# Performance work log

Measured on AMD Instinct MI355X. Metric: run time of the kernel, lower is better.

Reference implementation:

```python
import jax, jax.numpy as jnp
import numpy as np

N = 50000
E = 800000
DIN = 128
# SAGEConv layer dims: (in, out). conv0: input->embed; hidden: 128->64->128->256->512
DIMS = [(128, 128), (128, 64), (64, 128), (128, 256), (256, 512)]
NUM_CLASSES = 4


def setup_inputs() -> dict:
    key = jax.random.key(0)
    ks = jax.random.split(key, 3 * len(DIMS) + 4)
    inp = {"x": jax.random.normal(ks[0], (N, DIN), dtype=jnp.float32)}
    for i, (din, dout) in enumerate(DIMS):
        s = 1.0 / np.sqrt(din).astype(np.float32)
        inp[f"Wl{i}"] = jax.random.normal(ks[1 + 3 * i], (dout, din), dtype=jnp.float32) * s
        inp[f"bl{i}"] = jnp.zeros((dout,), dtype=jnp.float32)
        inp[f"Wr{i}"] = jax.random.normal(ks[2 + 3 * i], (dout, din), dtype=jnp.float32) * s
    dlast = DIMS[-1][1]
    inp["Wout"] = jax.random.normal(ks[-2], (NUM_CLASSES, dlast), dtype=jnp.float32) * (1.0 / np.sqrt(dlast).astype(np.float32))
    inp["bout"] = jnp.zeros((NUM_CLASSES,), dtype=jnp.float32)
    inp["edge_index"] = jax.random.randint(ks[-1], (2, E), 0, N, dtype=jnp.int32)
    return inp


def _forward(x, params, edge_index):
    src, dst = edge_index[0], edge_index[1]
    n = x.shape[0]
    # in-degree (count of incoming edges), clamped to >= 1 as in PyG mean aggregation
    deg = jax.ops.segment_sum(jnp.ones((src.shape[0],), x.dtype), dst, num_segments=n)
    deg_inv = (1.0 / jnp.maximum(deg, 1.0))[:, None]

    def sage(h, Wl, bl, Wr):
        # mean aggregation over incoming neighbors, then lin_l(agg) + lin_r(h)
        agg = jax.ops.segment_sum(h[src], dst, num_segments=n) * deg_inv
        return agg @ Wl.T + bl + h @ Wr.T

    h = x
    for i in range(len(DIMS)):
        h = jax.nn.relu(sage(h, params[f"Wl{i}"], params[f"bl{i}"], params[f"Wr{i}"]))
    logits = h @ params["Wout"].T + params["bout"]
    return jax.nn.softmax(logits, axis=-1)


def reference(x, Wl0, bl0, Wr0, Wl1, bl1, Wr1, Wl2, bl2, Wr2, Wl3, bl3, Wr3,
              Wl4, bl4, Wr4, Wout, bout, edge_index):
    params = {"Wl0": Wl0, "bl0": bl0, "Wr0": Wr0, "Wl1": Wl1, "bl1": bl1, "Wr1": Wr1,
              "Wl2": Wl2, "bl2": bl2, "Wr2": Wr2, "Wl3": Wl3, "bl3": bl3, "Wr3": Wr3,
              "Wl4": Wl4, "bl4": bl4, "Wr4": Wr4, "Wout": Wout, "bout": bout}
    return _forward(x, params, edge_index)
```

## Files before the change

kernel.cpp:

```cpp
#include <hip/hip_runtime.h>
#include <hip/hip_bf16.h>
#include <cstdint>
#include <cstddef>


typedef short bf16x8 __attribute__((ext_vector_type(8)));
typedef float f32x16 __attribute__((ext_vector_type(16)));

static inline int idiv_up(int a, int b) { return (a + b - 1) / b; }

static __device__ __forceinline__ float bf2f(unsigned short u) {
  union { unsigned int i; float f; } v; v.i = ((unsigned int)u) << 16; return v.f;
}
static __device__ __forceinline__ unsigned short f2bf(float f) {
  union { float f; unsigned int i; } v; v.f = f;
  return (unsigned short)((v.i + 0x7FFFu + ((v.i >> 16) & 1u)) >> 16);
}
static __device__ __forceinline__ float lo16(unsigned int u) { return bf2f((unsigned short)(u & 0xffffu)); }
static __device__ __forceinline__ float hi16(unsigned int u) { return bf2f((unsigned short)(u >> 16)); }
static __device__ __forceinline__ unsigned int packbf(float a, float b) {
  return (unsigned int)f2bf(a) | ((unsigned int)f2bf(b) << 16);
}

static __device__ __forceinline__ void gl_lds16(const void* g, void* l) {
  typedef __attribute__((address_space(3))) unsigned int lds_u32;
  typedef __attribute__((address_space(1))) const unsigned int glb_u32;
  __builtin_amdgcn_global_load_lds((glb_u32*)(uintptr_t)g,
                                   (lds_u32*)(unsigned int)(uintptr_t)l, 16, 0, 0);
}

__global__ void k_count_deg(const int* __restrict__ dst, int* __restrict__ deg, int E) {
  int e = blockIdx.x * blockDim.x + threadIdx.x;
  if (e < E) atomicAdd(deg + dst[e], 1);
}

__global__ __launch_bounds__(1024)
void k_scan(const int* __restrict__ deg, int* __restrict__ row_off, int* __restrict__ cursor,
            float* __restrict__ deg_inv, int n) {
  __shared__ int wsum[16];
  const int tid = threadIdx.x;
  const int lane = tid & 63, wid = tid >> 6;
  int carry = 0;
  for (int base = 0; base < n; base += 1024) {
    const int i = base + tid;
    const int v = (i < n) ? deg[i] : 0;
    int incl = v;
#pragma unroll
    for (int off = 1; off < 64; off <<= 1) {
      int t = __shfl_up(incl, off);
      if (lane >= off) incl += t;
    }
    if (lane == 63) wsum[wid] = incl;
    __syncthreads();
    if (wid == 0) {
      int wv = (lane < 16) ? wsum[lane] : 0;
#pragma unroll
      for (int off = 1; off < 16; off <<= 1) {
        int t = __shfl_up(wv, off);
        if (lane >= off) wv += t;
      }
      if (lane < 16) wsum[lane] = wv;
    }
    __syncthreads();
    const int woff = (wid > 0) ? wsum[wid - 1] : 0;
    if (i < n) {
      const int ro = carry + woff + incl - v;
      row_off[i] = ro;
      cursor[i] = ro;
      deg_inv[i] = 1.0f / (float)((v > 1) ? v : 1);
    }
    const int tot = wsum[15];
    __syncthreads();
    carry += tot;
  }
  if (tid == 0) row_off[n] = carry;
}

__global__ void k_fill_csr(const int* __restrict__ src, const int* __restrict__ dst,
                           int* __restrict__ cursor, int* __restrict__ esrc, int E) {
  int e = blockIdx.x * blockDim.x + threadIdx.x;
  if (e < E) {
    int d = dst[e];
    int p = atomicAdd(cursor + d, 1);
    esrc[p] = src[e];
  }
}

__global__ __launch_bounds__(256)
void k_conv_x(const float* __restrict__ src, unsigned short* __restrict__ dst, int n4) {
  for (int i = blockIdx.x * blockDim.x + threadIdx.x; i < n4; i += gridDim.x * blockDim.x) {
    const float4 v = *((const float4*)src + i);
    uint2 o;
    o.x = packbf(v.x, v.y);
    o.y = packbf(v.z, v.w);
    *((uint2*)dst + i) = o;
  }
}

struct PackJob { const float* src; unsigned short* dst; int O; int K; };
struct PackJobs { PackJob j[10]; };

__global__ __launch_bounds__(256)
void k_pack_w(PackJobs jobs) {
  const PackJob J = jobs.j[blockIdx.y];
  const int total = J.O * J.K / 2;
  const int OK64 = J.O * 64;
  for (int u = blockIdx.x * blockDim.x + threadIdx.x; u < total; u += gridDim.x * blockDim.x) {
    const int e = u * 2;
    const int kt = e / OK64;
    const int rem = e - kt * OK64;
    const int chunk = rem / (J.O * 8);
    const int rem2 = rem - chunk * (J.O * 8);
    const int col = rem2 >> 3;
    const int j = rem2 & 7;
    const int korig = kt * 64 + chunk * 8 + j;
    const float f0 = J.src[(size_t)col * J.K + korig];
    const float f1 = J.src[(size_t)col * J.K + korig + 1];
    ((unsigned int*)J.dst)[u] = packbf(f0, f1);
  }
}

static __device__ __forceinline__ void acc_u4(float* acc, const uint4& v) {
  acc[0] += lo16(v.x); acc[1] += hi16(v.x);
  acc[2] += lo16(v.y); acc[3] += hi16(v.y);
  acc[4] += lo16(v.z); acc[5] += hi16(v.z);
  acc[6] += lo16(v.w); acc[7] += hi16(v.w);
}

__global__ __launch_bounds__(256)
void k_agg128(const unsigned short* __restrict__ h, const int* __restrict__ row_off,
              const int* __restrict__ esrc, const float* __restrict__ deg_inv,
              unsigned short* __restrict__ agg, int N) {
  const int node = blockIdx.x * 4 + (threadIdx.x >> 6);
  if (node >= N) return;
  const int lane = threadIdx.x & 63;
  const int g = lane >> 4, c = lane & 15;
  const int s0 = row_off[node], s1 = row_off[node + 1];
  const uint4* hp = (const uint4*)h;
  float acc[8] = {0.f, 0.f, 0.f, 0.f, 0.f, 0.f, 0.f, 0.f};
  for (int i = s0; i < s1; i += 16) {
    int el = i + (lane & 15);
    if (el >= s1) el = s1 - 1;
    const int ev = esrc[el];
    uint4 v[4];
#pragma unroll
    for (int u = 0; u < 4; ++u) {
      if (i + u * 4 < s1) {
        const int e = __shfl(ev, u * 4 + g);
        v[u] = hp[(size_t)e * 16 + c];
      }
    }
#pragma unroll
    for (int u = 0; u < 4; ++u)
      if (i + u * 4 + g < s1) acc_u4(acc, v[u]);
  }
#pragma unroll
  for (int j = 0; j < 8; ++j) {
    acc[j] += __shfl_xor(acc[j], 16);
    acc[j] += __shfl_xor(acc[j], 32);
  }
  if (g == 0) {
    const float di = deg_inv[node];
    uint4 o;
    o.x = packbf(acc[0] * di, acc[1] * di);
    o.y = packbf(acc[2] * di, acc[3] * di);
    o.z = packbf(acc[4] * di, acc[5] * di);
    o.w = packbf(acc[6] * di, acc[7] * di);
    ((uint4*)agg)[(size_t)node * 16 + c] = o;
  }
}

__global__ __launch_bounds__(256)
void k_agg256(const unsigned short* __restrict__ h, const int* __restrict__ row_off,
              const int* __restrict__ esrc, const float* __restrict__ deg_inv,
              unsigned short* __restrict__ agg, int N) {
  const int node = blockIdx.x * 4 + (threadIdx.x >> 6);
  if (node >= N) return;
  const int lane = threadIdx.x & 63;
  const int g = lane >> 5, c = lane & 31;
  const int s0 = row_off[node], s1 = row_off[node + 1];
  const uint4* hp = (const uint4*)h;
  float acc[8] = {0.f, 0.f, 0.f, 0.f, 0.f, 0.f, 0.f, 0.f};
  for (int i = s0; i < s1; i += 16) {
    int el = i + (lane & 15);
    if (el >= s1) el = s1 - 1;
    const int ev = esrc[el];
    uint4 v[8];
#pragma unroll
    for (int u = 0; u < 8; ++u) {
      if (i + u * 2 < s1) {
        const int e = __shfl(ev, u * 2 + g);
        v[u] = hp[(size_t)e * 32 + c];
      }
    }
#pragma unroll
    for (int u = 0; u < 8; ++u)
      if (i + u * 2 + g < s1) acc_u4(acc, v[u]);
  }
#pragma unroll
  for (int j = 0; j < 8; ++j) acc[j] += __shfl_xor(acc[j], 32);
  if (g == 0) {
    const float di = deg_inv[node];
    uint4 o;
    o.x = packbf(acc[0] * di, acc[1] * di);
    o.y = packbf(acc[2] * di, acc[3] * di);
    o.z = packbf(acc[4] * di, acc[5] * di);
    o.w = packbf(acc[6] * di, acc[7] * di);
    ((uint4*)agg)[(size_t)node * 32 + c] = o;
  }
}

__global__ __launch_bounds__(256)
void k_agg64(const unsigned short* __restrict__ h, const int* __restrict__ row_off,
             const int* __restrict__ esrc, const float* __restrict__ deg_inv,
             unsigned short* __restrict__ agg, int N) {
  const int node = blockIdx.x * 4 + (threadIdx.x >> 6);
  if (node >= N) return;
  const int lane = threadIdx.x & 63;
  const int g = lane >> 3, c = lane & 7;
  const int s0 = row_off[node], s1 = row_off[node + 1];
  const uint4* hp = (const uint4*)h;
  float acc[8] = {0.f, 0.f, 0.f, 0.f, 0.f, 0.f, 0.f, 0.f};
  for (int i = s0; i < s1; i += 16) {
    int el = i + (lane & 15);
    if (el >= s1) el = s1 - 1;
    const int ev = esrc[el];
    uint4 v[2];
#pragma unroll
    for (int u = 0; u < 2; ++u) {
      if (i + u * 8 < s1) {
        const int e = __shfl(ev, u * 8 + g);
        v[u] = hp[(size_t)e * 8 + c];
      }
    }
#pragma unroll
    for (int u = 0; u < 2; ++u)
      if (i + u * 8 + g < s1) acc_u4(acc, v[u]);
  }
#pragma unroll
  for (int j = 0; j < 8; ++j) {
    acc[j] += __shfl_xor(acc[j], 8);
    acc[j] += __shfl_xor(acc[j], 16);
    acc[j] += __shfl_xor(acc[j], 32);
  }
  if (g == 0) {
    const float di = deg_inv[node];
    uint4 o;
    o.x = packbf(acc[0] * di, acc[1] * di);
    o.y = packbf(acc[2] * di, acc[3] * di);
    o.z = packbf(acc[4] * di, acc[5] * di);
    o.w = packbf(acc[6] * di, acc[7] * di);
    ((uint4*)agg)[(size_t)node * 8 + c] = o;
  }
}

template <int WC>
__global__ __launch_bounds__(WC * 128)
void k_sage_gemm(const unsigned short* __restrict__ A0, const unsigned short* __restrict__ B0,
                 const unsigned short* __restrict__ A1, const unsigned short* __restrict__ B1,
                 const float* __restrict__ bias, unsigned short* __restrict__ C,
                 int Nn, int K, int O) {
  constexpr int BN = WC * 64;
  constexpr int T = WC * 128;
  constexpr int ACH = 1024;
  constexpr int BCH = BN * 8;
  constexpr int LPT = (ACH + BCH) / T;
  constexpr int BSH = (WC == 1) ? 6 : ((WC == 2) ? 7 : 8);
  constexpr int LDSBUF = 16384 + BN * 128;
  __shared__ char lds[2 * LDSBUF];

  const int tid = threadIdx.x;
  const int w = tid >> 6, lane = tid & 63;
  const int wr = w / WC, wc = w % WC;
  const int fr = lane & 31, fq = lane >> 5;
  const int rowp = blockIdx.y;
  const int row0 = rowp * 128 + wr * 64;
  const int colb = blockIdx.x * BN;

  const int KT0 = K >> 6;
  const int NT = 2 * KT0;

  f32x16 acc[2][2];
#pragma unroll
  for (int m = 0; m < 2; ++m)
#pragma unroll
    for (int cn = 0; cn < 2; ++cn)
#pragma unroll
      for (int r = 0; r < 16; ++r) acc[m][cn][r] = 0.f;

  auto stage = [&](int buf, int t) {
    const int ph = (t >= KT0) ? 1 : 0;
    const unsigned short* Ab = ph ? A1 : A0;
    const unsigned short* Bb = ph ? B1 : B0;
    const int ktl = t - ph * KT0;
    char* lb = lds + buf * LDSBUF;
#pragma unroll
    for (int i = 0; i < LPT; ++i) {
      const int ch = tid + i * T;
      if (ch < ACH) {
        const int ar = ch >> 3, s = ch & 7;
        int g = rowp * 128 + ar;
        if (g >= Nn) g = Nn - 1;
        gl_lds16(Ab + (size_t)g * K + ktl * 64 + ((s ^ (ar & 7)) << 3), lb + ch * 16);
      } else {
        const int cb = ch - ACH;
        const int chunk = cb >> BSH, colrel = cb & (BN - 1);
        gl_lds16(Bb + (size_t)ktl * O * 64 + chunk * O * 8 + (colb + colrel) * 8,
                 lb + 16384 + cb * 16);
      }
    }
  };

  stage(0, 0);
#pragma unroll 1
  for (int t = 0; t < NT; ++t) {
    asm volatile("s_waitcnt vmcnt(0)" ::: "memory");
    __syncthreads();
    if (t + 1 < NT) stage((t + 1) & 1, t + 1);
    const char* lb = lds + (t & 1) * LDSBUF;
#pragma unroll
    for (int k16i = 0; k16i < 4; ++k16i) {
      const int c = k16i * 2 + fq;
      bf16x8 af[2], bg[2];
#pragma unroll
      for (int m = 0; m < 2; ++m) {
        const int rl = wr * 64 + m * 32 + fr;
        af[m] = *(const bf16x8*)(lb + rl * 128 + ((c ^ (rl & 7)) << 4));
      }
#pragma unroll
      for (int cn = 0; cn < 2; ++cn) {
        const int colrel = wc * 64 + cn * 32 + fr;
        bg[cn] = *(const bf16x8*)(lb + 16384 + c * (BN * 16) + colrel * 16);
      }
#pragma unroll
      for (int m = 0; m < 2; ++m)
#pragma unroll
        for (int cn = 0; cn < 2; ++cn)
          acc[m][cn] = __builtin_amdgcn_mfma_f32_32x32x16_bf16(af[m], bg[cn], acc[m][cn], 0, 0, 0);
    }
  }

#pragma unroll
  for (int cn = 0; cn < 2; ++cn) {
    const int col = colb + wc * 64 + cn * 32 + fr;
    const float bb = bias[col];
#pragma unroll
    for (int m = 0; m < 2; ++m) {
#pragma unroll
      for (int reg = 0; reg < 16; ++reg) {
        const float v = fmaxf(acc[m][cn][reg] + bb, 0.f);
        const float nb = __shfl_xor(v, 1);
        const int row = row0 + m * 32 + (reg & 3) + 8 * (reg >> 2) + 4 * fq;
        if (!(lane & 1) && row < Nn) {
          *(unsigned int*)(C + (size_t)row * O + col) = packbf(v, nb);
        }
      }
    }
  }
}

__global__ __launch_bounds__(256)
void k_out_softmax(const unsigned short* __restrict__ h, const float* __restrict__ W4,
                   const float* __restrict__ b, float* __restrict__ out, int N) {
  const int n = blockIdx.x * 4 + (threadIdx.x >> 6);
  if (n >= N) return;
  const int lane = threadIdx.x & 63;
  const unsigned int* hp = (const unsigned int*)h + (size_t)n * 256;
  float a[4] = {0.f, 0.f, 0.f, 0.f};
#pragma unroll
  for (int it = 0; it < 4; ++it) {
    const unsigned int v = hp[it * 64 + lane];
    const float lo = lo16(v);
    const float hi = hi16(v);
    const int k = (it * 64 + lane) * 2;
#pragma unroll
    for (int c = 0; c < 4; ++c)
      a[c] += lo * W4[c * 512 + k] + hi * W4[c * 512 + k + 1];
  }
#pragma unroll
  for (int off = 32; off > 0; off >>= 1) {
#pragma unroll
    for (int c = 0; c < 4; ++c) a[c] += __shfl_down(a[c], off);
  }
  if (lane == 0) {
    const float l0 = a[0] + b[0], l1 = a[1] + b[1], l2 = a[2] + b[2], l3 = a[3] + b[3];
    const float m = fmaxf(fmaxf(l0, l1), fmaxf(l2, l3));
    const float e0 = expf(l0 - m), e1 = expf(l1 - m), e2 = expf(l2 - m), e3 = expf(l3 - m);
    const float inv = 1.0f / (e0 + e1 + e2 + e3);
    float4 r; r.x = e0 * inv; r.y = e1 * inv; r.z = e2 * inv; r.w = e3 * inv;
    *(float4*)(out + (size_t)n * 4) = r;
  }
}

extern "C" void kernel_launch(void* const* d_in, const int* in_sizes, int n_in,
                              void* d_out, int out_size, void* d_ws, size_t ws_size,
                              hipStream_t stream) {
  const float* x = (const float*)d_in[0];
  const float* Wl[5] = {(const float*)d_in[1], (const float*)d_in[4], (const float*)d_in[7],
                        (const float*)d_in[10], (const float*)d_in[13]};
  const float* bl[5] = {(const float*)d_in[2], (const float*)d_in[5], (const float*)d_in[8],
                        (const float*)d_in[11], (const float*)d_in[14]};
  const float* Wr[5] = {(const float*)d_in[3], (const float*)d_in[6], (const float*)d_in[9],
                        (const float*)d_in[12], (const float*)d_in[15]};
  const float* Wout = (const float*)d_in[16];
  const float* bout = (const float*)d_in[17];
  const int* eidx = (const int*)d_in[18];

  const int N = in_sizes[0] / 128;
  const int E = in_sizes[18] / 2;
  const int* srcI = eidx;
  const int* dstI = eidx + E;

  const int Kd[5] = {128, 128, 64, 128, 256};
  const int Od[5] = {128, 64, 128, 256, 512};

  char* ws = (char*)d_ws;
  size_t p = 0;
  auto alloc = [&](size_t bytes) { size_t r = p; p += (bytes + 255) & ~(size_t)255; return r; };
  int*   deg     = (int*)(ws + alloc((size_t)N * 4));
  int*   row_off = (int*)(ws + alloc((size_t)(N + 1) * 4));
  int*   cursor  = (int*)(ws + alloc((size_t)N * 4));
  float* deg_inv = (float*)(ws + alloc((size_t)N * 4));
  int*   esrc    = (int*)(ws + alloc((size_t)E * 4));
  unsigned short* xb = (unsigned short*)(ws + alloc((size_t)N * 128 * 2));
  unsigned short* wlb[5];
  unsigned short* wrb[5];
  for (int l = 0; l < 5; ++l) {
    wlb[l] = (unsigned short*)(ws + alloc((size_t)Od[l] * Kd[l] * 2));
    wrb[l] = (unsigned short*)(ws + alloc((size_t)Od[l] * Kd[l] * 2));
  }
  unsigned short* bufA = (unsigned short*)(ws + alloc((size_t)N * 512 * 2));
  unsigned short* bufB = (unsigned short*)(ws + alloc((size_t)N * 256 * 2));
  unsigned short* agg  = (unsigned short*)(ws + alloc((size_t)N * 256 * 2));
  (void)ws_size; (void)n_in; (void)out_size;

  k_conv_x<<<128, 256, 0, stream>>>(x, xb, N * 128 / 4);
  PackJobs jobs;
  for (int l = 0; l < 5; ++l) {
    jobs.j[2 * l]     = {Wl[l], wlb[l], Od[l], Kd[l]};
    jobs.j[2 * l + 1] = {Wr[l], wrb[l], Od[l], Kd[l]};
  }
  k_pack_w<<<dim3(32, 10), 256, 0, stream>>>(jobs);

  hipMemsetAsync(deg, 0, (size_t)N * 4, stream);
  k_count_deg<<<idiv_up(E, 256), 256, 0, stream>>>(dstI, deg, E);
  k_scan<<<1, 1024, 0, stream>>>(deg, row_off, cursor, deg_inv, N);
  k_fill_csr<<<idiv_up(E, 256), 256, 0, stream>>>(srcI, dstI, cursor, esrc, E);

  unsigned short* houts[5] = {bufA, bufB, bufA, bufB, bufA};

  const unsigned short* hin = xb;
  const int gx = idiv_up(N, 128);
  for (int l = 0; l < 5; ++l) {
    const int K = Kd[l], O = Od[l];
    if (K == 64)
      k_agg64<<<idiv_up(N, 4), 256, 0, stream>>>(hin, row_off, esrc, deg_inv, agg, N);
    else if (K == 128)
      k_agg128<<<idiv_up(N, 4), 256, 0, stream>>>(hin, row_off, esrc, deg_inv, agg, N);
    else
      k_agg256<<<idiv_up(N, 4), 256, 0, stream>>>(hin, row_off, esrc, deg_inv, agg, N);

    unsigned short* hout = houts[l];
    switch (l) {
      case 0:
        k_sage_gemm<2><<<dim3(1, gx), 256, 0, stream>>>(agg, wlb[l], hin, wrb[l], bl[l], hout, N, K, O);
        break;
      case 1:
        k_sage_gemm<1><<<dim3(1, gx), 128, 0, stream>>>(agg, wlb[l], hin, wrb[l], bl[l], hout, N, K, O);
        break;
      case 2:
        k_sage_gemm<2><<<dim3(1, gx), 256, 0, stream>>>(agg, wlb[l], hin, wrb[l], bl[l], hout, N, K, O);
        break;
      case 3:
        k_sage_gemm<2><<<dim3(2, gx), 256, 0, stream>>>(agg, wlb[l], hin, wrb[l], bl[l], hout, N, K, O);
        break;
      default:
        k_sage_gemm<2><<<dim3(4, gx), 256, 0, stream>>>(agg, wlb[l], hin, wrb[l], bl[l], hout, N, K, O);
        break;
    }
    hin = hout;
  }
  k_out_softmax<<<idiv_up(N, 4), 256, 0, stream>>>(hin, Wout, bout, (float*)d_out, N);
}
```

Measured before the change: 465.3 us.

## Reorder layer 1 to transform-then-aggregate and remap GEMM blocks for L2 locality

For the 128->64 layer, the code now multiplies h by the concatenated [Wl|Wr] weights first, producing a 128-wide intermediate. A new fused kernel then aggregates the 64-wide Wl·h half over neighbours, scales by deg_inv, and adds the Wr·h half, bias and ReLU. This halves the gathered feature width for that layer, at the cost of an extra GEMM output round trip and bf16 rounding of the pre-aggregated product. The GEMM grid also becomes 1D with a swizzle that groups 8 row tiles across all column blocks, aiming to improve reuse of the A tiles in L2.

```diff
diff --git a/kernel.cpp b/kernel.cpp
--- a/kernel.cpp
+++ b/kernel.cpp
@@ -97,26 +97,22 @@
   }
 }
 
-struct PackJob { const float* src; unsigned short* dst; int O; int K; };
+struct PackJob { const float* src; unsigned short* dst; int O; int K; int colOff; int Opack; };
 struct PackJobs { PackJob j[10]; };
 
 __global__ __launch_bounds__(256)
 void k_pack_w(PackJobs jobs) {
   const PackJob J = jobs.j[blockIdx.y];
   const int total = J.O * J.K / 2;
-  const int OK64 = J.O * 64;
   for (int u = blockIdx.x * blockDim.x + threadIdx.x; u < total; u += gridDim.x * blockDim.x) {
     const int e = u * 2;
-    const int kt = e / OK64;
-    const int rem = e - kt * OK64;
-    const int chunk = rem / (J.O * 8);
-    const int rem2 = rem - chunk * (J.O * 8);
-    const int col = rem2 >> 3;
-    const int j = rem2 & 7;
-    const int korig = kt * 64 + chunk * 8 + j;
-    const float f0 = J.src[(size_t)col * J.K + korig];
-    const float f1 = J.src[(size_t)col * J.K + korig + 1];
-    ((unsigned int*)J.dst)[u] = packbf(f0, f1);
+    const int col = e / J.K;
+    const int k = e - col * J.K;
+    const int kt = k >> 6, ch = (k >> 3) & 7, j = k & 7;
+    const float f0 = J.src[(size_t)col * J.K + k];
+    const float f1 = J.src[(size_t)col * J.K + k + 1];
+    const int didx = kt * (J.Opack * 64) + ch * (J.Opack * 8) + (col + J.colOff) * 8 + j;
+    ((unsigned int*)J.dst)[didx >> 1] = packbf(f0, f1);
   }
 }
 
@@ -254,7 +250,59 @@
   }
 }
 
-template <int WC>
+__global__ __launch_bounds__(256)
+void k_agg_post64(const unsigned short* __restrict__ z, const int* __restrict__ row_off,
+                  const int* __restrict__ esrc, const float* __restrict__ deg_inv,
+                  const float* __restrict__ bias, unsigned short* __restrict__ out, int N) {
+  const int node = blockIdx.x * 4 + (threadIdx.x >> 6);
+  if (node >= N) return;
+  const int lane = threadIdx.x & 63;
+  const int g = lane >> 3, c = lane & 7;
+  const int s0 = row_off[node], s1 = row_off[node + 1];
+  const uint4* zp = (const uint4*)z;
+  float acc[8] = {0.f, 0.f, 0.f, 0.f, 0.f, 0.f, 0.f, 0.f};
+  for (int i = s0; i < s1; i += 16) {
+    int el = i + (lane & 15);
+    if (el >= s1) el = s1 - 1;
+    const int ev = esrc[el];
+    uint4 v[2];
+#pragma unroll
+    for (int u = 0; u < 2; ++u) {
+      if (i + u * 8 < s1) {
+        const int e = __shfl(ev, u * 8 + g);
+        v[u] = zp[(size_t)e * 16 + c];
+      }
+    }
+#pragma unroll
+    for (int u = 0; u < 2; ++u)
+      if (i + u * 8 + g < s1) acc_u4(acc, v[u]);
+  }
+#pragma unroll
+  for (int j = 0; j < 8; ++j) {
+    acc[j] += __shfl_xor(acc[j], 8);
+    acc[j] += __shfl_xor(acc[j], 16);
+    acc[j] += __shfl_xor(acc[j], 32);
+  }
+  if (g == 0) {
+    const float di = deg_inv[node];
+    const uint4 yr = zp[(size_t)node * 16 + 8 + c];
+    float y[8];
+    y[0] = lo16(yr.x); y[1] = hi16(yr.x); y[2] = lo16(yr.y); y[3] = hi16(yr.y);
+    y[4] = lo16(yr.z); y[5] = hi16(yr.z); y[6] = lo16(yr.w); y[7] = hi16(yr.w);
+    float r[8];
+#pragma unroll
+    for (int j = 0; j < 8; ++j)
+      r[j] = fmaxf(acc[j] * di + y[j] + bias[c * 8 + j], 0.f);
+    uint4 o;
+    o.x = packbf(r[0], r[1]);
+    o.y = packbf(r[2], r[3]);
+    o.z = packbf(r[4], r[5]);
+    o.w = packbf(r[6], r[7]);
+    ((uint4*)out)[(size_t)node * 8 + c] = o;
+  }
+}
+
+template <int WC, int NCB, bool FUSED>
 __global__ __launch_bounds__(WC * 128)
 void k_sage_gemm(const unsigned short* __restrict__ A0, const unsigned short* __restrict__ B0,
                  const unsigned short* __restrict__ A1, const unsigned short* __restrict__ B1,
@@ -269,16 +317,23 @@
   constexpr int LDSBUF = 16384 + BN * 128;
   __shared__ char lds[2 * LDSBUF];
 
+  const int nrp = (Nn + 127) >> 7;
+  const int bid = blockIdx.x;
+  const int r8 = bid & 7;
+  const int tb = bid >> 3;
+  const int cb = tb % NCB;
+  const int rowp = (tb / NCB) * 8 + r8;
+  if (rowp >= nrp) return;
+
   const int tid = threadIdx.x;
   const int w = tid >> 6, lane = tid & 63;
   const int wr = w / WC, wc = w % WC;
   const int fr = lane & 31, fq = lane >> 5;
-  const int rowp = blockIdx.y;
   const int row0 = rowp * 128 + wr * 64;
-  const int colb = blockIdx.x * BN;
+  const int colb = cb * BN;
 
   const int KT0 = K >> 6;
-  const int NT = 2 * KT0;
+  const int NT = FUSED ? 2 * KT0 : KT0;
 
   f32x16 acc[2][2];
 #pragma unroll
@@ -289,10 +344,17 @@
       for (int r = 0; r < 16; ++r) acc[m][cn][r] = 0.f;
 
   auto stage = [&](int buf, int t) {
-    const int ph = (t >= KT0) ? 1 : 0;
-    const unsigned short* Ab = ph ? A1 : A0;
-    const unsigned short* Bb = ph ? B1 : B0;
-    const int ktl = t - ph * KT0;
+    const unsigned short* Ab;
+    const unsigned short* Bb;
+    int ktl;
+    if (FUSED) {
+      const int ph = (t >= KT0) ? 1 : 0;
+      Ab = ph ? A1 : A0;
+      Bb = ph ? B1 : B0;
+      ktl = t - ph * KT0;
+    } else {
+      Ab = A0; Bb = B0; ktl = t;
+    }
     char* lb = lds + buf * LDSBUF;
 #pragma unroll
     for (int i = 0; i < LPT; ++i) {
@@ -303,10 +365,10 @@
         if (g >= Nn) g = Nn - 1;
         gl_lds16(Ab + (size_t)g * K + ktl * 64 + ((s ^ (ar & 7)) << 3), lb + ch * 16);
       } else {
-        const int cb = ch - ACH;
-        const int chunk = cb >> BSH, colrel = cb & (BN - 1);
+        const int cbch = ch - ACH;
+        const int chunk = cbch >> BSH, colrel = cbch & (BN - 1);
         gl_lds16(Bb + (size_t)ktl * O * 64 + chunk * O * 8 + (colb + colrel) * 8,
-                 lb + 16384 + cb * 16);
+                 lb + 16384 + cbch * 16);
       }
     }
   };
@@ -343,12 +405,14 @@
 #pragma unroll
   for (int cn = 0; cn < 2; ++cn) {
     const int col = colb + wc * 64 + cn * 32 + fr;
-    const float bb = bias[col];
+    float bb = 0.f;
+    if (FUSED) bb = bias[col];
 #pragma unroll
     for (int m = 0; m < 2; ++m) {
 #pragma unroll
       for (int reg = 0; reg < 16; ++reg) {
-        const float v = fmaxf(acc[m][cn][reg] + bb, 0.f);
+        float v = acc[m][cn][reg];
+        if (FUSED) v = fmaxf(v + bb, 0.f);
         const float nb = __shfl_xor(v, 1);
         const int row = row0 + m * 32 + (reg & 3) + 8 * (reg >> 2) + 4 * fq;
         if (!(lane & 1) && row < Nn) {
@@ -429,6 +493,7 @@
     wlb[l] = (unsigned short*)(ws + alloc((size_t)Od[l] * Kd[l] * 2));
     wrb[l] = (unsigned short*)(ws + alloc((size_t)Od[l] * Kd[l] * 2));
   }
+  unsigned short* wcat1 = (unsigned short*)(ws + alloc((size_t)128 * 128 * 2));
   unsigned short* bufA = (unsigned short*)(ws + alloc((size_t)N * 512 * 2));
   unsigned short* bufB = (unsigned short*)(ws + alloc((size_t)N * 256 * 2));
   unsigned short* agg  = (unsigned short*)(ws + alloc((size_t)N * 256 * 2));
@@ -437,8 +502,13 @@
   k_conv_x<<<128, 256, 0, stream>>>(x, xb, N * 128 / 4);
   PackJobs jobs;
   for (int l = 0; l < 5; ++l) {
-    jobs.j[2 * l]     = {Wl[l], wlb[l], Od[l], Kd[l]};
-    jobs.j[2 * l + 1] = {Wr[l], wrb[l], Od[l], Kd[l]};
+    if (l == 1) {
+      jobs.j[2] = {Wl[1], wcat1, 64, 128, 0, 128};
+      jobs.j[3] = {Wr[1], wcat1, 64, 128, 64, 128};
+    } else {
+      jobs.j[2 * l]     = {Wl[l], wlb[l], Od[l], Kd[l], 0, Od[l]};
+      jobs.j[2 * l + 1] = {Wr[l], wrb[l], Od[l], Kd[l], 0, Od[l]};
+    }
   }
   k_pack_w<<<dim3(32, 10), 256, 0, stream>>>(jobs);
 
@@ -447,38 +517,22 @@
   k_scan<<<1, 1024, 0, stream>>>(deg, row_off, cursor, deg_inv, N);
   k_fill_csr<<<idiv_up(E, 256), 256, 0, stream>>>(srcI, dstI, cursor, esrc, E);
 
-  unsigned short* houts[5] = {bufA, bufB, bufA, bufB, bufA};
-
-  const unsigned short* hin = xb;
-  const int gx = idiv_up(N, 128);
-  for (int l = 0; l < 5; ++l) {
-    const int K = Kd[l], O = Od[l];
-    if (K == 64)
-      k_agg64<<<idiv_up(N, 4), 256, 0, stream>>>(hin, row_off, esrc, deg_inv, agg, N);
-    else if (K == 128)
-      k_agg128<<<idiv_up(N, 4), 256, 0, stream>>>(hin, row_off, esrc, deg_inv, agg, N);
-    else
-      k_agg256<<<idiv_up(N, 4), 256, 0, stream>>>(hin, row_off, esrc, deg_inv, agg, N);
-
-    unsigned short* hout = houts[l];
-    switch (l) {
-      case 0:
-        k_sage_gemm<2><<<dim3(1, gx), 256, 0, stream>>>(agg, wlb[l], hin, wrb[l], bl[l], hout, N, K, O);
-        break;
-      case 1:
-        k_sage_gemm<1><<<dim3(1, gx), 128, 0, stream>>>(agg, wlb[l], hin, wrb[l], bl[l], hout, N, K, O);
-        break;
-      case 2:
-        k_sage_gemm<2><<<dim3(1, gx), 256, 0, stream>>>(agg, wlb[l], hin, wrb[l], bl[l], hout, N, K, O);
-        break;
-      case 3:
-        k_sage_gemm<2><<<dim3(2, gx), 256, 0, stream>>>(agg, wlb[l], hin, wrb[l], bl[l], hout, N, K, O);
-        break;
-      default:
-        k_sage_gemm<2><<<dim3(4, gx), 256, 0, stream>>>(agg, wlb[l], hin, wrb[l], bl[l], hout, N, K, O);
-        break;
-    }
-    hin = hout;
-  }
-  k_out_softmax<<<idiv_up(N, 4), 256, 0, stream>>>(hin, Wout, bout, (float*)d_out, N);
-}
+  const int gx8 = 8 * ((idiv_up(N, 128) + 7) / 8);
+
+  k_agg128<<<idiv_up(N, 4), 256, 0, stream>>>(xb, row_off, esrc, deg_inv, agg, N);
+  k_sage_gemm<2, 1, true><<<gx8, 256, 0, stream>>>(agg, wlb[0], xb, wrb[0], bl[0], bufA, N, 128, 128);
+
+  k_sage_gemm<2, 1, false><<<gx8, 256, 0, stream>>>(bufA, wcat1, bufA, wcat1, bl[1], agg, N, 128, 128);
+  k_agg_post64<<<idiv_up(N, 4), 256, 0, stream>>>(agg, row_off, esrc, deg_inv, bl[1], bufB, N);
+
+  k_agg64<<<idiv_up(N, 4), 256, 0, stream>>>(bufB, row_off, esrc, deg_inv, agg, N);
+  k_sage_gemm<2, 1, true><<<gx8, 256, 0, stream>>>(agg, wlb[2], bufB, wrb[2], bl[2], bufA, N, 64, 128);
+
+  k_agg128<<<idiv_up(N, 4), 256, 0, stream>>>(bufA, row_off, esrc, deg_inv, agg, N);
+  k_sage_gemm<2, 2, true><<<2 * gx8, 256, 0, stream>>>(agg, wlb[3], bufA, wrb[3], bl[3], bufB, N, 128, 256);
+
+  k_agg256<<<idiv_up(N, 4), 256, 0, stream>>>(bufB, row_off, esrc, deg_inv, agg, N);
+  k_sage_gemm<2, 4, true><<<4 * gx8, 256, 0, stream>>>(agg, wlb[4], bufB, wrb[4], bl[4], bufA, N, 256, 512);
+
+  k_out_softmax<<<idiv_up(N, 4), 256, 0, stream>>>(bufA, Wout, bout, (float*)d_out, N);
+}
```

Result: no change. 461.9 us (-0.7%).
